# Kernel tuning notes

Hardware: AMD Instinct MI355X
Metric: run time of the kernel (lower is better)

## Reference

```python
import jax, jax.numpy as jnp
import numpy as np

DIM_H = 128
N_EXPERTS = 4
N_GRAPHS = 256
EPS = 1e-5


def setup_inputs() -> dict:
    key = jax.random.key(0)
    ks = jax.random.split(key, 16)
    N, E, D = 100000, 1600000, DIM_H
    x = jax.random.normal(ks[0], (N, D), dtype=jnp.float32)
    edge_index = jax.random.randint(ks[1], (2, E), 0, N, dtype=jnp.int64)
    batch = jnp.sort(jax.random.randint(ks[2], (N,), 0, N_GRAPHS, dtype=jnp.int64))
    s = 0.05
    gin = 2 * D + 4  # router input: mean | max | 4 graph stats
    params = dict(
        temperature=jnp.ones((1,), jnp.float32) * 2.0,
        rw1=jax.random.normal(ks[3], (gin, D), jnp.float32) * s,
        rb1=jnp.zeros((D,), jnp.float32),
        rw2=jax.random.normal(ks[4], (D, D // 2), jnp.float32) * s,
        rb2=jnp.zeros((D // 2,), jnp.float32),
        rw3=jax.random.normal(ks[5], (D // 2, N_EXPERTS), jnp.float32) * s,
        rb3=jnp.zeros((N_EXPERTS,), jnp.float32),
        expert_w=jax.random.normal(ks[6], (N_EXPERTS, D, D), jnp.float32) * s,
        expert_b=jnp.zeros((N_EXPERTS, D), jnp.float32),
        bn1_g=jnp.ones((D,), jnp.float32),
        bn1_b=jnp.zeros((D,), jnp.float32),
        ff_w1=jax.random.normal(ks[7], (D, 2 * D), jnp.float32) * s,
        ff_b1=jnp.zeros((2 * D,), jnp.float32),
        ff_w2=jax.random.normal(ks[8], (2 * D, D), jnp.float32) * s,
        ff_b2=jnp.zeros((D,), jnp.float32),
        bn2_g=jnp.ones((D,), jnp.float32),
        bn2_b=jnp.zeros((D,), jnp.float32),
    )
    return dict(x=x, edge_index=edge_index, batch=batch, **params)


def _gcn_agg(x, src, dst, n):
    deg = jnp.zeros((n,), x.dtype).at[dst].add(1.0) + 1.0
    dinv = jax.lax.rsqrt(deg)
    coef = dinv[src] * dinv[dst]                        # [E]
    agg = jax.ops.segment_sum(x[src] * coef[:, None], dst, num_segments=n)
    return agg + x * (1.0 / deg)[:, None]               # self-loop term (coef = 1/deg)


def _batchnorm(h, g, b):
    mu = jnp.mean(h, axis=0)
    var = jnp.var(h, axis=0)
    return (h - mu) * jax.lax.rsqrt(var + EPS) * g + b


def reference(x, edge_index, batch, temperature, rw1, rb1, rw2, rb2, rw3, rb3,
              expert_w, expert_b, bn1_g, bn1_b, ff_w1, ff_b1, ff_w2, ff_b2,
              bn2_g, bn2_b):
    n = x.shape[0]
    src, dst = edge_index[0], edge_index[1]
    B = N_GRAPHS

    # ---- graph embeddings: [mean_pool | max_pool | 4 stats] -> [B, 2D+4] ----
    cnt = jnp.maximum(jax.ops.segment_sum(jnp.ones((n,), x.dtype), batch, num_segments=B), 1.0)
    gmean = jax.ops.segment_sum(x, batch, num_segments=B) / cnt[:, None]
    gmax = jax.ops.segment_max(x, batch, num_segments=B)
    node_deg = jnp.zeros((n,), x.dtype).at[dst].add(1.0)
    mean_deg = jax.ops.segment_sum(node_deg, batch, num_segments=B) / cnt
    max_deg = jax.ops.segment_max(node_deg, batch, num_segments=B)
    stats = jnp.stack([cnt, mean_deg, max_deg, jnp.log(cnt)], axis=-1)  # [B,4]
    ge = jnp.concatenate([gmean, gmax, stats], axis=-1)

    # ---- router: MLP + temperature softmax -> [B, E] ----
    h = jax.nn.relu(ge @ rw1 + rb1)
    h = jax.nn.relu(h @ rw2 + rb2)
    scores = h @ rw3 + rb3
    gates = jax.nn.softmax(scores / temperature, axis=-1)   # [B, n_experts]

    # ---- experts: GCNConv_i(x). Aggregation is linear so do it once. ----
    agg = _gcn_agg(x, src, dst, n)                          # [N, D]
    expert_out = jnp.einsum('nd,edo->neo', agg, expert_w) + expert_b[None]  # [N,E,D]

    # ---- softmax-gated combine with per-graph gates ----
    kv = jnp.einsum('neo,ne->no', expert_out, gates[batch])  # [N, D]

    # ---- residual + batchnorm + FFN block ----
    kv = _batchnorm(x + kv, bn1_g, bn1_b)
    ff = jax.nn.relu(kv @ ff_w1 + ff_b1) @ ff_w2 + ff_b2
    out = _batchnorm(kv + ff, bn2_g, bn2_b)
    return out
```

## Files before the change

kernel.cpp:

```cpp
#include <hip/hip_runtime.h>
#include <math.h>

#define D 128
#define B 256
#define EPSV 1e-5f
#define NREP 64

typedef __attribute__((ext_vector_type(8))) short short8;
typedef __attribute__((ext_vector_type(4))) float f32x4;

static __device__ __forceinline__ ushort f2bf(float f) {
  union { float f; unsigned u; } v; v.f = f;
  unsigned r = (v.u + 0x7fffu + ((v.u >> 16) & 1u)) >> 16;
  return (ushort)r;
}
static __device__ __forceinline__ float bf2f(ushort u) {
  union { unsigned u; float f; } v; v.u = ((unsigned)u) << 16; return v.f;
}
static __device__ __forceinline__ float uaf(unsigned u) {
  union { unsigned u; float f; } v; v.u = u; return v.f;
}
static __device__ __forceinline__ unsigned encf(float f) {
  union { float f; unsigned u; } v; v.f = f;
  return (v.u & 0x80000000u) ? ~v.u : (v.u | 0x80000000u);
}
static __device__ __forceinline__ float decf(unsigned e) {
  union { unsigned u; float f; } v;
  v.u = (e & 0x80000000u) ? (e & 0x7FFFFFFFu) : ~e;
  return v.f;
}
#define ENC_NEGINF 0x007FFFFFu

static __global__ void __launch_bounds__(256) setup_kernel(
    int* bcnt, float* bn1s, float* bn1s2, float* bn2s, float* bn2s2,
    float* gsum, unsigned* gmaxE, float* gcnt, float* gdsum, unsigned* gdmaxE,
    const float* __restrict__ w1, const float* __restrict__ w2,
    ushort* __restrict__ w1t, ushort* __restrict__ w2t,
    int N, int nbInit) {
  int b = blockIdx.x, t = threadIdx.x;
  if (b < nbInit) {
    int i = b * 256 + t;
    if (i < 256) bcnt[i] = 0;
    if (i < NREP * D) { bn1s[i] = 0.f; bn1s2[i] = 0.f; bn2s[i] = 0.f; bn2s2[i] = 0.f; }
    if (i < B * D) { gsum[i] = 0.f; gmaxE[i] = ENC_NEGINF; }
    if (i < B) { gcnt[i] = 0.f; gdsum[i] = 0.f; gdmaxE[i] = ENC_NEGINF; }
  } else {
    int i = (b - nbInit) * 256 + t;
    { int j = i >> 7, d = i & 127; w1t[i] = f2bf(w1[(size_t)d * 256 + j]); }
    { int o = i >> 8, j = i & 255; w2t[i] = f2bf(w2[(size_t)j * 128 + o]); }
  }
}

static __global__ void __launch_bounds__(256) bhist_kernel(
    const int* __restrict__ dst, int* bcnt, int E) {
  __shared__ int histS[256];
  int t = threadIdx.x;
  int base = blockIdx.x * 4096;
  histS[t] = 0;
  __syncthreads();
#pragma unroll
  for (int k = 0; k < 16; k++) {
    int e = base + k * 256 + t;
    if (e < E) atomicAdd(&histS[dst[e] >> 9], 1);
  }
  __syncthreads();
  int hv = histS[t];
  if (hv > 0) atomicAdd(&bcnt[t], hv);
}

static __global__ void bscan_kernel(const int* __restrict__ bcnt, int* bbase, int* bcur) {
  __shared__ int sS[256];
  int t = threadIdx.x;
  int v = bcnt[t];
  sS[t] = v; __syncthreads();
  for (int off = 1; off < 256; off <<= 1) {
    int add = (t >= off) ? sS[t - off] : 0;
    __syncthreads();
    sS[t] += add;
    __syncthreads();
  }
  int incl = sS[t];
  bbase[t + 1] = incl;
  bcur[t] = incl - v;
  if (t == 0) bbase[0] = 0;
}

static __global__ void statspart_kernel(const float* __restrict__ x, const int* __restrict__ batch,
                                        const float* __restrict__ dinv,
                                        float* gsum, unsigned* gmaxE,
                                        ushort* __restrict__ x_bf, int N) {
  __shared__ float dS[32];
  __shared__ int bSg[32];
  int t = threadIdx.x;
  int n0 = blockIdx.x * 32;
  int nend = min(n0 + 32, N);
  int nn = nend - n0;
  if (t < 32) {
    int n = min(n0 + t, N - 1);
    dS[t] = dinv[n];
    bSg[t] = batch[n];
  }
  __syncthreads();
  float v[32];
#pragma unroll
  for (int k = 0; k < 32; k++)
    v[k] = (k < nn) ? x[(size_t)(n0 + k) * D + t] : 0.f;
#pragma unroll
  for (int k = 0; k < 32; k++)
    if (k < nn) x_bf[(size_t)(n0 + k) * D + t] = f2bf(v[k] * dS[k]);
  int curg = bSg[0];
  float s = 0.f, mx = -INFINITY;
#pragma unroll
  for (int k = 0; k < 32; k++) {
    if (k < nn) {
      int g = bSg[k];
      if (g != curg) {
        atomicAdd(&gsum[curg * D + t], s);
        atomicMax(&gmaxE[curg * D + t], encf(mx));
        s = 0.f; mx = -INFINITY; curg = g;
      }
      s += v[k]; mx = fmaxf(mx, v[k]);
    }
  }
  atomicAdd(&gsum[curg * D + t], s);
  atomicMax(&gmaxE[curg * D + t], encf(mx));
}

static __global__ void router_kernel(
    const float* __restrict__ gsum, const unsigned* __restrict__ gmaxE,
    const float* __restrict__ gcnt, const float* __restrict__ gdsum,
    const unsigned* __restrict__ gdmaxE,
    const float* __restrict__ rw1, const float* __restrict__ rb1,
    const float* __restrict__ rw2, const float* __restrict__ rb2,
    const float* __restrict__ rw3, const float* __restrict__ rb3,
    const float* __restrict__ temp, float* __restrict__ gates) {
  int g = blockIdx.x, t = threadIdx.x;
  __shared__ float geS[260], h1S[D], h2S[64], scS[4];
  float cntf = fmaxf(gcnt[g], 1.f);
  geS[t] = gsum[g * D + t] / cntf;
  geS[D + t] = decf(gmaxE[g * D + t]);
  if (t == 0) {
    geS[256] = cntf;
    geS[257] = gdsum[g] / cntf;
    geS[258] = decf(gdmaxE[g]);
    geS[259] = logf(cntf);
  }
  __syncthreads();
  float a = rb1[t];
  for (int k = 0; k < 260; k++) a += geS[k] * rw1[k * D + t];
  h1S[t] = fmaxf(a, 0.f);
  __syncthreads();
  if (t < 64) { float b = rb2[t]; for (int k = 0; k < D; k++) b += h1S[k] * rw2[k * 64 + t]; h2S[t] = fmaxf(b, 0.f); }
  __syncthreads();
  if (t < 4) { float c = rb3[t]; for (int k = 0; k < 64; k++) c += h2S[k] * rw3[k * 4 + t]; scS[t] = c; }
  __syncthreads();
  if (t == 0) {
    float T = temp[0];
    float q0 = scS[0] / T, q1 = scS[1] / T, q2 = scS[2] / T, q3 = scS[3] / T;
    float m = fmaxf(fmaxf(q0, q1), fmaxf(q2, q3));
    float e0 = expf(q0 - m), e1 = expf(q1 - m), e2 = expf(q2 - m), e3 = expf(q3 - m);
    float inv = 1.f / (e0 + e1 + e2 + e3);
    gates[g * 4 + 0] = e0 * inv; gates[g * 4 + 1] = e1 * inv;
    gates[g * 4 + 2] = e2 * inv; gates[g * 4 + 3] = e3 * inv;
  }
}

static __global__ void __launch_bounds__(256) wcomb_kernel(
    const float* __restrict__ gates, const float* __restrict__ ew,
    const float* __restrict__ eb, ushort* __restrict__ W_combT,
    float* __restrict__ b_comb) {
  __shared__ ushort wS[128 * 130];
  int g = blockIdx.x, t = threadIdx.x;
  float g0 = gates[g * 4], g1 = gates[g * 4 + 1], g2 = gates[g * 4 + 2], g3 = gates[g * 4 + 3];
  for (int k = t; k < D * D; k += 256) {
    int d = k >> 7, o = k & 127;
    float v = g0 * ew[k] + g1 * ew[16384 + k] + g2 * ew[32768 + k] + g3 * ew[49152 + k];
    wS[o * 130 + d] = f2bf(v);
  }
  __syncthreads();
  for (int k = t; k < D * D; k += 256) {
    int o = k >> 7, d = k & 127;
    W_combT[(size_t)g * 16384 + k] = wS[o * 130 + d];
  }
  if (t < D)
    b_comb[g * D + t] = g0 * eb[t] + g1 * eb[D + t] + g2 * eb[2 * D + t] + g3 * eb[3 * D + t];
}

static __global__ void __launch_bounds__(256) fillA_kernel(
    const int* __restrict__ src, const int* __restrict__ dst,
    int* bcur, int* __restrict__ esort, int E) {
  __shared__ int histS[256], startS[256], cursorS[256], gbaseS[256];
  __shared__ int eS[4096];
  __shared__ unsigned char bS[4096];
  int t = threadIdx.x;
  int base = blockIdx.x * 4096;
  int cnt = min(4096, E - base);
  int srcR[16], dstR[16];
  histS[t] = 0;
  __syncthreads();
#pragma unroll
  for (int k = 0; k < 16; k++) {
    int e = base + k * 256 + t;
    if (e < E) { srcR[k] = src[e]; dstR[k] = dst[e]; }
    else dstR[k] = -1;
  }
#pragma unroll
  for (int k = 0; k < 16; k++)
    if (dstR[k] >= 0) atomicAdd(&histS[dstR[k] >> 9], 1);
  __syncthreads();
  int hv = histS[t];
  startS[t] = hv;
  __syncthreads();
  for (int off = 1; off < 256; off <<= 1) {
    int add = (t >= off) ? startS[t - off] : 0;
    __syncthreads();
    startS[t] += add;
    __syncthreads();
  }
  int excl = startS[t] - hv;
  __syncthreads();
  startS[t] = excl;
  cursorS[t] = excl;
  gbaseS[t] = (hv > 0) ? atomicAdd(&bcur[t], hv) : 0;
  __syncthreads();
#pragma unroll
  for (int k = 0; k < 16; k++)
    if (dstR[k] >= 0) {
      int b = dstR[k] >> 9;
      int p = atomicAdd(&cursorS[b], 1);
      eS[p] = (srcR[k] << 9) | (dstR[k] & 511);
      bS[p] = (unsigned char)b;
    }
  __syncthreads();
  for (int k = t; k < cnt; k += 256) {
    int b = bS[k];
    esort[gbaseS[b] + (k - startS[b])] = eS[k];
  }
}

static __global__ void __launch_bounds__(256) fillB_kernel(
    const int* __restrict__ esort, const int* __restrict__ bbase,
    int* __restrict__ rowoff, int* __restrict__ node_deg, float* __restrict__ dinv,
    int* __restrict__ csr_src, int N) {
  __shared__ int degS[512];
  __shared__ int pS[256];
  __shared__ int curS[512];
  int b = blockIdx.x, t = threadIdx.x;
  int n0 = b << 9, n1 = min(n0 + 512, N);
  int nn = n1 - n0;
  int r0 = bbase[b], r1 = bbase[b + 1];
  degS[t] = 0; degS[t + 256] = 0;
  __syncthreads();
  for (int e = r0 + t; e < r1; e += 256) atomicAdd(&degS[esort[e] & 511], 1);
  __syncthreads();
  int d0 = degS[2 * t], d1 = degS[2 * t + 1];
  int ps = d0 + d1;
  pS[t] = ps;
  __syncthreads();
  for (int off = 1; off < 256; off <<= 1) {
    int add = (t >= off) ? pS[t - off] : 0;
    __syncthreads();
    pS[t] += add;
    __syncthreads();
  }
  int pexcl = pS[t] - ps;
  int e0 = pexcl, e1 = pexcl + d0;
  curS[2 * t] = r0 + e0;
  curS[2 * t + 1] = r0 + e1;
  int i0 = 2 * t, i1 = 2 * t + 1;
  if (i0 < nn) {
    rowoff[n0 + i0 + 1] = r0 + e0 + d0;
    node_deg[n0 + i0] = d0;
    dinv[n0 + i0] = rsqrtf((float)d0 + 1.f);
  }
  if (i1 < nn) {
    rowoff[n0 + i1 + 1] = r0 + e1 + d1;
    node_deg[n0 + i1] = d1;
    dinv[n0 + i1] = rsqrtf((float)d1 + 1.f);
  }
  if (b == 0 && t == 0) rowoff[0] = 0;
  __syncthreads();
  for (int e = r0 + t; e < r1; e += 256) {
    int v = esort[e];
    int p = atomicAdd(&curS[v & 511], 1);
    csr_src[p] = v >> 9;
  }
}

static __global__ void nodestats_kernel(const int* __restrict__ node_deg,
                                        const int* __restrict__ batch,
                                        float* gcnt, float* gdsum, unsigned* gdmaxE, int N) {
  int i = blockIdx.x * 256 + threadIdx.x;
  int nd = (i < N) ? node_deg[i] : 0;
  int g = batch[min(i, N - 1)];
  float dv = (float)nd;
  int g0w = __shfl(g, 0);
  int waveLast = blockIdx.x * 256 + ((threadIdx.x >> 6) << 6) + 63;
  bool uni = (waveLast < N) && __all(g == g0w);
  if (uni) {
    float s = dv, mx = dv;
    for (int off = 32; off > 0; off >>= 1) { s += __shfl_down(s, off); mx = fmaxf(mx, __shfl_down(mx, off)); }
    if ((threadIdx.x & 63) == 0) {
      atomicAdd(&gcnt[g0w], 64.f);
      atomicAdd(&gdsum[g0w], s);
      atomicMax(&gdmaxE[g0w], encf(mx));
    }
  } else if (i < N) {
    atomicAdd(&gcnt[g], 1.f);
    atomicAdd(&gdsum[g], dv);
    atomicMax(&gdmaxE[g], encf(dv));
  }
}

static __global__ void __launch_bounds__(256) gather_kernel(
    const ushort* __restrict__ xb, const int* __restrict__ rowoff,
    const int* __restrict__ csr_src, const float* __restrict__ dinv,
    ushort* __restrict__ aggB, int N) {
  __shared__ int eS[4][64];
  int t = threadIdx.x, w = t >> 6, l = t & 63;
  int n = blockIdx.x * 4 + w;
  if (n >= N) return;
  int h = l >> 4;
  int c16 = l & 15;
  int r0 = rowoff[n], r1 = rowoff[n + 1];
  float dn = dinv[n];
  const uint4* xb4 = (const uint4*)xb;
  uint4 xo = xb4[(size_t)n * 16 + c16];
  float acc[8];
#pragma unroll
  for (int i = 0; i < 8; i++) acc[i] = 0.f;
  int pads = 0;
#define ACC8(v) { \
    unsigned u0 = (v).x, u1 = (v).y, u2 = (v).z, u3 = (v).w; \
    acc[0] += uaf(u0 << 16); acc[1] += uaf(u0 & 0xFFFF0000u); \
    acc[2] += uaf(u1 << 16); acc[3] += uaf(u1 & 0xFFFF0000u); \
    acc[4] += uaf(u2 << 16); acc[5] += uaf(u2 & 0xFFFF0000u); \
    acc[6] += uaf(u3 << 16); acc[7] += uaf(u3 & 0xFFFF0000u); }
  for (int j0 = r0; j0 < r1; j0 += 64) {
    int cnt = min(64, r1 - j0);
    int cnt4 = (cnt + 3) & ~3;
    pads += cnt4 - cnt;
    eS[w][l] = (j0 + l < r1) ? csr_src[j0 + l] : n;
    int k = 0;
    for (; k + 16 <= cnt4; k += 16) {
      int s0 = eS[w][k + h];
      int s1 = eS[w][k + 4 + h];
      int s2 = eS[w][k + 8 + h];
      int s3 = eS[w][k + 12 + h];
      uint4 v0 = xb4[(size_t)s0 * 16 + c16];
      uint4 v1 = xb4[(size_t)s1 * 16 + c16];
      uint4 v2 = xb4[(size_t)s2 * 16 + c16];
      uint4 v3 = xb4[(size_t)s3 * 16 + c16];
      ACC8(v0); ACC8(v1); ACC8(v2); ACC8(v3);
    }
    if (k + 8 <= cnt4) {
      int s0 = eS[w][k + h];
      int s1 = eS[w][k + 4 + h];
      uint4 v0 = xb4[(size_t)s0 * 16 + c16];
      uint4 v1 = xb4[(size_t)s1 * 16 + c16];
      ACC8(v0); ACC8(v1);
      k += 8;
    }
    if (k < cnt4) {
      int s0 = eS[w][k + h];
      uint4 v0 = xb4[(size_t)s0 * 16 + c16];
      ACC8(v0);
    }
  }
#undef ACC8
#pragma unroll
  for (int i = 0; i < 8; i++) {
    acc[i] += __shfl_down(acc[i], 32);
    acc[i] += __shfl_down(acc[i], 16);
  }
  if (l < 16) {
    float wn = 1.f - (float)pads;
    float xf[8];
    xf[0] = uaf(xo.x << 16); xf[1] = uaf(xo.x & 0xFFFF0000u);
    xf[2] = uaf(xo.y << 16); xf[3] = uaf(xo.y & 0xFFFF0000u);
    xf[4] = uaf(xo.z << 16); xf[5] = uaf(xo.z & 0xFFFF0000u);
    xf[6] = uaf(xo.w << 16); xf[7] = uaf(xo.w & 0xFFFF0000u);
    unsigned o[4];
#pragma unroll
    for (int i = 0; i < 4; i++) {
      unsigned lo = f2bf(dn * (acc[2 * i] + wn * xf[2 * i]));
      unsigned hi = f2bf(dn * (acc[2 * i + 1] + wn * xf[2 * i + 1]));
      o[i] = lo | (hi << 16);
    }
    uint4 ov; ov.x = o[0]; ov.y = o[1]; ov.z = o[2]; ov.w = o[3];
    ((uint4*)aggB)[(size_t)n * 16 + c16] = ov;
  }
}

static __global__ void __launch_bounds__(256) expert_kernel(
    const ushort* __restrict__ aggB, const float* __restrict__ x, const int* __restrict__ batch,
    const ushort* __restrict__ W_combT, const float* __restrict__ b_comb,
    ushort* __restrict__ hB, float* bn1s, float* bn1s2, int N) {
  __shared__ __align__(16) ushort aggS[64 * 136];
  __shared__ __align__(16) ushort wS[128 * 136];
  __shared__ int bS[64];
  int t = threadIdx.x;
  int nwg = gridDim.x;
  int q = nwg >> 3, r = nwg & 7;
  int xcd = blockIdx.x & 7, ix = blockIdx.x >> 3;
  int tilei = (xcd < r) ? (xcd * (q + 1) + ix) : (r * (q + 1) + (xcd - r) * q + ix);
  int n0 = tilei * 64;
  int tile = min(64, N - n0);
  for (int k = t; k < 64 * 16; k += 256) {
    int i = k >> 4, c = (k & 15) * 8;
    short8 v = (short8){0, 0, 0, 0, 0, 0, 0, 0};
    if (i < tile) v = *(const short8*)&aggB[(size_t)(n0 + i) * D + c];
    *(short8*)&aggS[i * 136 + c] = v;
  }
  if (t < 64) bS[t] = batch[min(n0 + t, N - 1)];
  __syncthreads();
  int w = t >> 6, ln = t & 15, quad = (t & 63) >> 4, l64 = t & 63;
  int myg = bS[l64];
  int gnext = __shfl_down(myg, 1);
  unsigned long long bmask = __ballot(l64 == 63 || myg != gnext);
  float s[2] = {0.f, 0.f}, s2[2] = {0.f, 0.f};
  int mstart = 0;
  while (mstart < tile) {
    int g = __shfl(myg, mstart);
    int mend = mstart + __ffsll((unsigned long long)(bmask >> mstart));
    if (mend > tile) mend = tile;
    __syncthreads();
    const ushort* Wg = W_combT + (size_t)g * 16384;
    for (int k = t; k < 128 * 16; k += 256) {
      int o = k >> 4, c = (k & 15) * 8;
      *(short8*)&wS[o * 136 + c] = *(const short8*)&Wg[(size_t)o * 128 + c];
    }
    __syncthreads();
    f32x4 acc[4][2];
#pragma unroll
    for (int mi = 0; mi < 4; mi++)
#pragma unroll
      for (int ni = 0; ni < 2; ni++) acc[mi][ni] = (f32x4){0.f, 0.f, 0.f, 0.f};
#pragma unroll
    for (int ks = 0; ks < 4; ks++) {
      int kk = ks * 32 + quad * 8;
      short8 a[4], b[2];
#pragma unroll
      for (int mi = 0; mi < 4; mi++) a[mi] = *(const short8*)&aggS[(mi * 16 + ln) * 136 + kk];
#pragma unroll
      for (int ni = 0; ni < 2; ni++) b[ni] = *(const short8*)&wS[(w * 32 + ni * 16 + ln) * 136 + kk];
#pragma unroll
      for (int mi = 0; mi < 4; mi++)
#pragma unroll
        for (int ni = 0; ni < 2; ni++)
          acc[mi][ni] = __builtin_amdgcn_mfma_f32_16x16x32_bf16(a[mi], b[ni], acc[mi][ni], 0, 0, 0);
    }
    float bias[2];
#pragma unroll
    for (int ni = 0; ni < 2; ni++) bias[ni] = b_comb[g * D + w * 32 + ni * 16 + ln];
#pragma unroll
    for (int mi = 0; mi < 4; mi++)
#pragma unroll
      for (int r2_ = 0; r2_ < 4; r2_++) {
        int m = mi * 16 + quad * 4 + r2_;
        if (m >= mstart && m < mend) {
          size_t rowoff_ = (size_t)(n0 + m) * D;
#pragma unroll
          for (int ni = 0; ni < 2; ni++) {
            int o = w * 32 + ni * 16 + ln;
            float hv = x[rowoff_ + o] + acc[mi][ni][r2_] + bias[ni];
            hB[rowoff_ + o] = f2bf(hv);
            s[ni] += hv; s2[ni] += hv * hv;
          }
        }
      }
    mstart = mend;
  }
#pragma unroll
  for (int ni = 0; ni < 2; ni++) {
    s[ni] += __shfl_down(s[ni], 32);  s[ni] += __shfl_down(s[ni], 16);
    s2[ni] += __shfl_down(s2[ni], 32); s2[ni] += __shfl_down(s2[ni], 16);
  }
  if (quad == 0) {
    int slot = (tilei & (NREP - 1)) * D;
#pragma unroll
    for (int ni = 0; ni < 2; ni++) {
      int o = w * 32 + ni * 16 + ln;
      atomicAdd(&bn1s[slot + o], s[ni]);
      atomicAdd(&bn1s2[slot + o], s2[ni]);
    }
  }
}

static __global__ void bnfin_kernel(const float* s, const float* s2,
                                    const float* __restrict__ g, const float* __restrict__ b,
                                    float* sc, float* sh, float invN) {
  int t = threadIdx.x;
  if (t < D) {
    float st = 0.f, s2t = 0.f;
    for (int k = 0; k < NREP; k++) { st += s[k * D + t]; s2t += s2[k * D + t]; }
    float m = st * invN;
    float var = s2t * invN - m * m;
    float rstd = rsqrtf(var + EPSV);
    float scv = rstd * g[t];
    sc[t] = scv;
    sh[t] = b[t] - m * scv;
  }
}

static __global__ void __launch_bounds__(512, 4) ffn_kernel(
    ushort* __restrict__ hB, const float* __restrict__ sc1, const float* __restrict__ sh1,
    const ushort* __restrict__ w1t, const float* __restrict__ fb1,
    const ushort* __restrict__ w2t, const float* __restrict__ fb2,
    float* bn2s, float* bn2s2, int N) {
  __shared__ __align__(16) ushort kvnS[64 * 136];
  __shared__ __align__(16) ushort hidS[64 * 264];
  int t = threadIdx.x, n0 = blockIdx.x * 64;
  int tile = min(64, N - n0);
  for (int k = t; k < 64 * 16; k += 512) {
    int i = k >> 4, c = (k & 15) * 8;
    ushort o[8];
    if (i < tile) {
      uint4 hv = *(const uint4*)&hB[(size_t)(n0 + i) * D + c];
      unsigned uu[4] = {hv.x, hv.y, hv.z, hv.w};
#pragma unroll
      for (int j = 0; j < 4; j++) {
        float lo = uaf(uu[j] << 16) * sc1[c + 2 * j] + sh1[c + 2 * j];
        float hi = uaf(uu[j] & 0xFFFF0000u) * sc1[c + 2 * j + 1] + sh1[c + 2 * j + 1];
        o[2 * j] = f2bf(lo); o[2 * j + 1] = f2bf(hi);
      }
    } else {
#pragma unroll
      for (int j = 0; j < 8; j++) o[j] = 0;
    }
    *(short8*)&kvnS[i * 136 + c] = *(short8*)o;
  }
  __syncthreads();
  int w = t >> 6, ln = t & 15, quad = (t & 63) >> 4;
  f32x4 acc1[4][2];
#pragma unroll
  for (int mi = 0; mi < 4; mi++)
#pragma unroll
    for (int ni = 0; ni < 2; ni++) acc1[mi][ni] = (f32x4){0.f, 0.f, 0.f, 0.f};
#pragma unroll
  for (int ks = 0; ks < 4; ks++) {
    int kk = ks * 32 + quad * 8;
    short8 a[4], b[2];
#pragma unroll
    for (int mi = 0; mi < 4; mi++) a[mi] = *(const short8*)&kvnS[(mi * 16 + ln) * 136 + kk];
#pragma unroll
    for (int ni = 0; ni < 2; ni++) b[ni] = *(const short8*)&w1t[(size_t)(w * 32 + ni * 16 + ln) * 128 + kk];
#pragma unroll
    for (int mi = 0; mi < 4; mi++)
#pragma unroll
      for (int ni = 0; ni < 2; ni++)
        acc1[mi][ni] = __builtin_amdgcn_mfma_f32_16x16x32_bf16(a[mi], b[ni], acc1[mi][ni], 0, 0, 0);
  }
  float bias1[2];
#pragma unroll
  for (int ni = 0; ni < 2; ni++) bias1[ni] = fb1[w * 32 + ni * 16 + ln];
#pragma unroll
  for (int mi = 0; mi < 4; mi++)
#pragma unroll
    for (int ni = 0; ni < 2; ni++)
#pragma unroll
      for (int r = 0; r < 4; r++) {
        int mrow = mi * 16 + quad * 4 + r;
        int j = w * 32 + ni * 16 + ln;
        hidS[mrow * 264 + j] = f2bf(fmaxf(acc1[mi][ni][r] + bias1[ni], 0.f));
      }
  __syncthreads();
  int o = w * 16 + ln;
  f32x4 acc2[4];
#pragma unroll
  for (int mi = 0; mi < 4; mi++) acc2[mi] = (f32x4){0.f, 0.f, 0.f, 0.f};
#pragma unroll
  for (int ks = 0; ks < 8; ks++) {
    int kk = ks * 32 + quad * 8;
    short8 a[4], b;
#pragma unroll
    for (int mi = 0; mi < 4; mi++) a[mi] = *(const short8*)&hidS[(mi * 16 + ln) * 264 + kk];
    b = *(const short8*)&w2t[(size_t)o * 256 + kk];
#pragma unroll
    for (int mi = 0; mi < 4; mi++)
      acc2[mi] = __builtin_amdgcn_mfma_f32_16x16x32_bf16(a[mi], b, acc2[mi], 0, 0, 0);
  }
  float bias2 = fb2[o];
  float s = 0.f, s2 = 0.f;
#pragma unroll
  for (int mi = 0; mi < 4; mi++)
#pragma unroll
    for (int r = 0; r < 4; r++) {
      int mrow = mi * 16 + quad * 4 + r;
      if (mrow < tile) {
        size_t ro = (size_t)(n0 + mrow) * D;
        float v = bf2f(kvnS[mrow * 136 + o]) + acc2[mi][r] + bias2;
        hB[ro + o] = f2bf(v);
        s += v; s2 += v * v;
      }
    }
  s += __shfl_down(s, 32);  s += __shfl_down(s, 16);
  s2 += __shfl_down(s2, 32); s2 += __shfl_down(s2, 16);
  if (quad == 0) {
    int slot = (blockIdx.x & (NREP - 1)) * D;
    atomicAdd(&bn2s[slot + o], s);
    atomicAdd(&bn2s2[slot + o], s2);
  }
}

static __global__ void bnapply_kernel(const ushort* __restrict__ hB, float* __restrict__ out,
                                      const float* __restrict__ sc, const float* __restrict__ sh,
                                      int total8) {
  int i = blockIdx.x * 256 + threadIdx.x;
  if (i < total8) {
    int c = (i * 8) & 127;
    uint4 hv = ((const uint4*)hB)[i];
    unsigned uu[4] = {hv.x, hv.y, hv.z, hv.w};
    float4 o0, o1;
    o0.x = uaf(uu[0] << 16) * sc[c] + sh[c];
    o0.y = uaf(uu[0] & 0xFFFF0000u) * sc[c + 1] + sh[c + 1];
    o0.z = uaf(uu[1] << 16) * sc[c + 2] + sh[c + 2];
    o0.w = uaf(uu[1] & 0xFFFF0000u) * sc[c + 3] + sh[c + 3];
    o1.x = uaf(uu[2] << 16) * sc[c + 4] + sh[c + 4];
    o1.y = uaf(uu[2] & 0xFFFF0000u) * sc[c + 5] + sh[c + 5];
    o1.z = uaf(uu[3] << 16) * sc[c + 6] + sh[c + 6];
    o1.w = uaf(uu[3] & 0xFFFF0000u) * sc[c + 7] + sh[c + 7];
    ((float4*)out)[i * 2] = o0;
    ((float4*)out)[i * 2 + 1] = o1;
  }
}

extern "C" void kernel_launch(void* const* d_in, const int* in_sizes, int n_in,
                              void* d_out, int out_size, void* d_ws, size_t ws_size,
                              hipStream_t stream) {
  (void)n_in; (void)out_size; (void)ws_size;
  const float* x    = (const float*)d_in[0];
  const int*   ei   = (const int*)d_in[1];
  const int*   batch= (const int*)d_in[2];
  const float* temp = (const float*)d_in[3];
  const float* rw1  = (const float*)d_in[4];
  const float* rb1  = (const float*)d_in[5];
  const float* rw2  = (const float*)d_in[6];
  const float* rb2  = (const float*)d_in[7];
  const float* rw3  = (const float*)d_in[8];
  const float* rb3  = (const float*)d_in[9];
  const float* ew   = (const float*)d_in[10];
  const float* eb   = (const float*)d_in[11];
  const float* bn1g = (const float*)d_in[12];
  const float* bn1b = (const float*)d_in[13];
  const float* fw1  = (const float*)d_in[14];
  const float* fb1  = (const float*)d_in[15];
  const float* fw2  = (const float*)d_in[16];
  const float* fb2  = (const float*)d_in[17];
  const float* bn2g = (const float*)d_in[18];
  const float* bn2b = (const float*)d_in[19];

  int N = in_sizes[0] / D;
  int E = in_sizes[1] / 2;
  const int* src = ei;
  const int* dst = ei + E;

  ushort* x_bf = (ushort*)d_out;
  ushort* aggB = (ushort*)((char*)d_out + (size_t)N * D * 2);

  char* p = (char*)d_ws;
  auto alloc = [&](size_t bytes) -> void* {
    void* r = (void*)p;
    p += (bytes + 255) & ~(size_t)255;
    return r;
  };
  int NB = (N + 511) >> 9;
  int*   node_deg = (int*)alloc((size_t)N * 4);
  int*   rowoff   = (int*)alloc(((size_t)N + 1) * 4);
  int*   csr_src  = (int*)alloc((size_t)E * 4);
  int*   esort    = (int*)alloc((size_t)E * 4);
  int*   bcnt     = (int*)alloc(256 * 4);
  int*   bbase    = (int*)alloc(257 * 4);
  int*   bcur     = (int*)alloc(256 * 4);
  float* dinv     = (float*)alloc((size_t)N * 4);
  ushort* hB      = (ushort*)alloc((size_t)N * D * 2);
  float* gsum     = (float*)alloc((size_t)B * D * 4);
  unsigned* gmaxE = (unsigned*)alloc((size_t)B * D * 4);
  float* gcnt     = (float*)alloc((size_t)B * 4);
  float* gdsum    = (float*)alloc((size_t)B * 4);
  unsigned* gdmaxE= (unsigned*)alloc((size_t)B * 4);
  float* gates    = (float*)alloc((size_t)B * 4 * 4);
  float* b_comb   = (float*)alloc((size_t)B * D * 4);
  float* bn1s     = (float*)alloc((size_t)NREP * D * 4);
  float* bn1s2    = (float*)alloc((size_t)NREP * D * 4);
  float* sc1      = (float*)alloc(D * 4);
  float* sh1      = (float*)alloc(D * 4);
  float* bn2s     = (float*)alloc((size_t)NREP * D * 4);
  float* bn2s2    = (float*)alloc((size_t)NREP * D * 4);
  float* sc2      = (float*)alloc(D * 4);
  float* sh2      = (float*)alloc(D * 4);
  ushort* W_combT = (ushort*)alloc((size_t)B * D * D * 2);
  ushort* w1t     = (ushort*)alloc((size_t)D * 256 * 2);
  ushort* w2t     = (ushort*)alloc((size_t)D * 256 * 2);

  int nbInit = (N + 255) / 256;
  setup_kernel<<<nbInit + 128, 256, 0, stream>>>(
      bcnt, bn1s, bn1s2, bn2s, bn2s2, gsum, gmaxE, gcnt, gdsum, gdmaxE,
      fw1, fw2, w1t, w2t, N, nbInit);
  bhist_kernel<<<(E + 4095) / 4096, 256, 0, stream>>>(dst, bcnt, E);
  bscan_kernel<<<1, 256, 0, stream>>>(bcnt, bbase, bcur);
  fillA_kernel<<<(E + 4095) / 4096, 256, 0, stream>>>(src, dst, bcur, esort, E);
  fillB_kernel<<<NB, 256, 0, stream>>>(esort, bbase, rowoff, node_deg, dinv, csr_src, N);
  nodestats_kernel<<<(N + 255) / 256, 256, 0, stream>>>(node_deg, batch, gcnt, gdsum, gdmaxE, N);
  statspart_kernel<<<(N + 31) / 32, 128, 0, stream>>>(x, batch, dinv, gsum, gmaxE, x_bf, N);
  router_kernel<<<B, 128, 0, stream>>>(gsum, gmaxE, gcnt, gdsum, gdmaxE,
                                       rw1, rb1, rw2, rb2, rw3, rb3, temp, gates);
  wcomb_kernel<<<B, 256, 0, stream>>>(gates, ew, eb, W_combT, b_comb);
  gather_kernel<<<(N + 3) / 4, 256, 0, stream>>>(x_bf, rowoff, csr_src, dinv, aggB, N);
  int nb64 = (N + 63) / 64;
  expert_kernel<<<nb64, 256, 0, stream>>>(aggB, x, batch, W_combT, b_comb, hB, bn1s, bn1s2, N);
  bnfin_kernel<<<1, 128, 0, stream>>>(bn1s, bn1s2, bn1g, bn1b, sc1, sh1, 1.0f / (float)N);
  ffn_kernel<<<nb64, 512, 0, stream>>>(hB, sc1, sh1, w1t, fb1, w2t, fb2, bn2s, bn2s2, N);
  bnfin_kernel<<<1, 128, 0, stream>>>(bn2s, bn2s2, bn2g, bn2b, sc2, sh2, 1.0f / (float)N);
  int total8 = N * D / 8;
  bnapply_kernel<<<(total8 + 255) / 256, 256, 0, stream>>>(hB, (float*)d_out, sc2, sh2, total8);
}
```

Measured before the change: 416.7 us.

## Fuse per-graph degree stats into fillB and split FFN hidden into halves

Removes the separate nodestats kernel by computing per-graph count, degree sum and max degree inside fillB, which already holds each node's degree, using wave-level reductions when a wave maps to a single graph. The FFN kernel now processes the 256-wide hidden layer in two 128-column halves, accumulating the second GEMM across halves. This halves the hidden LDS buffer and raises the launch-bounds occupancy target from 4 to 8 blocks, at the cost of an extra barrier per half and possible register pressure.

```diff
diff --git a/kernel.cpp b/kernel.cpp
--- a/kernel.cpp
+++ b/kernel.cpp
@@ -241,7 +241,8 @@
 static __global__ void __launch_bounds__(256) fillB_kernel(
     const int* __restrict__ esort, const int* __restrict__ bbase,
     int* __restrict__ rowoff, int* __restrict__ node_deg, float* __restrict__ dinv,
-    int* __restrict__ csr_src, int N) {
+    int* __restrict__ csr_src, const int* __restrict__ batch,
+    float* gcnt, float* gdsum, unsigned* gdmaxE, int N) {
   __shared__ int degS[512];
   __shared__ int pS[256];
   __shared__ int curS[512];
@@ -279,36 +280,36 @@
     dinv[n0 + i1] = rsqrtf((float)d1 + 1.f);
   }
   if (b == 0 && t == 0) rowoff[0] = 0;
+  {
+    bool v0 = i0 < nn, v1 = i1 < nn;
+    int gn0 = batch[min(n0 + i0, N - 1)];
+    int gn1 = batch[min(n0 + i1, N - 1)];
+    int gfirst = __shfl(gn0, 0);
+    bool uni = __all(gn0 == gfirst) && __all(gn1 == gfirst);
+    if (uni) {
+      float cnt = (v0 ? 1.f : 0.f) + (v1 ? 1.f : 0.f);
+      float sum = (v0 ? (float)d0 : 0.f) + (v1 ? (float)d1 : 0.f);
+      float mx = fmaxf(v0 ? (float)d0 : -INFINITY, v1 ? (float)d1 : -INFINITY);
+      for (int off = 32; off > 0; off >>= 1) {
+        cnt += __shfl_down(cnt, off);
+        sum += __shfl_down(sum, off);
+        mx = fmaxf(mx, __shfl_down(mx, off));
+      }
+      if ((t & 63) == 0 && cnt > 0.f) {
+        atomicAdd(&gcnt[gfirst], cnt);
+        atomicAdd(&gdsum[gfirst], sum);
+        atomicMax(&gdmaxE[gfirst], encf(mx));
+      }
+    } else {
+      if (v0) { atomicAdd(&gcnt[gn0], 1.f); atomicAdd(&gdsum[gn0], (float)d0); atomicMax(&gdmaxE[gn0], encf((float)d0)); }
+      if (v1) { atomicAdd(&gcnt[gn1], 1.f); atomicAdd(&gdsum[gn1], (float)d1); atomicMax(&gdmaxE[gn1], encf((float)d1)); }
+    }
+  }
   __syncthreads();
   for (int e = r0 + t; e < r1; e += 256) {
     int v = esort[e];
     int p = atomicAdd(&curS[v & 511], 1);
     csr_src[p] = v >> 9;
-  }
-}
-
-static __global__ void nodestats_kernel(const int* __restrict__ node_deg,
-                                        const int* __restrict__ batch,
-                                        float* gcnt, float* gdsum, unsigned* gdmaxE, int N) {
-  int i = blockIdx.x * 256 + threadIdx.x;
-  int nd = (i < N) ? node_deg[i] : 0;
-  int g = batch[min(i, N - 1)];
-  float dv = (float)nd;
-  int g0w = __shfl(g, 0);
-  int waveLast = blockIdx.x * 256 + ((threadIdx.x >> 6) << 6) + 63;
-  bool uni = (waveLast < N) && __all(g == g0w);
-  if (uni) {
-    float s = dv, mx = dv;
-    for (int off = 32; off > 0; off >>= 1) { s += __shfl_down(s, off); mx = fmaxf(mx, __shfl_down(mx, off)); }
-    if ((threadIdx.x & 63) == 0) {
-      atomicAdd(&gcnt[g0w], 64.f);
-      atomicAdd(&gdsum[g0w], s);
-      atomicMax(&gdmaxE[g0w], encf(mx));
-    }
-  } else if (i < N) {
-    atomicAdd(&gcnt[g], 1.f);
-    atomicAdd(&gdsum[g], dv);
-    atomicMax(&gdmaxE[g], encf(dv));
   }
 }
 
@@ -503,13 +504,13 @@
   }
 }
 
-static __global__ void __launch_bounds__(512, 4) ffn_kernel(
+static __global__ void __launch_bounds__(512, 8) ffn_kernel(
     ushort* __restrict__ hB, const float* __restrict__ sc1, const float* __restrict__ sh1,
     const ushort* __restrict__ w1t, const float* __restrict__ fb1,
     const ushort* __restrict__ w2t, const float* __restrict__ fb2,
     float* bn2s, float* bn2s2, int N) {
   __shared__ __align__(16) ushort kvnS[64 * 136];
-  __shared__ __align__(16) ushort hidS[64 * 264];
+  __shared__ __align__(16) ushort hidS[64 * 136];
   int t = threadIdx.x, n0 = blockIdx.x * 64;
   int tile = min(64, N - n0);
   for (int k = t; k < 64 * 16; k += 512) {
@@ -532,53 +533,47 @@
   }
   __syncthreads();
   int w = t >> 6, ln = t & 15, quad = (t & 63) >> 4;
-  f32x4 acc1[4][2];
-#pragma unroll
-  for (int mi = 0; mi < 4; mi++)
-#pragma unroll
-    for (int ni = 0; ni < 2; ni++) acc1[mi][ni] = (f32x4){0.f, 0.f, 0.f, 0.f};
-#pragma unroll
-  for (int ks = 0; ks < 4; ks++) {
-    int kk = ks * 32 + quad * 8;
-    short8 a[4], b[2];
-#pragma unroll
-    for (int mi = 0; mi < 4; mi++) a[mi] = *(const short8*)&kvnS[(mi * 16 + ln) * 136 + kk];
-#pragma unroll
-    for (int ni = 0; ni < 2; ni++) b[ni] = *(const short8*)&w1t[(size_t)(w * 32 + ni * 16 + ln) * 128 + kk];
+  int o = w * 16 + ln;
+  f32x4 acc2[4];
+#pragma unroll
+  for (int mi = 0; mi < 4; mi++) acc2[mi] = (f32x4){0.f, 0.f, 0.f, 0.f};
+#pragma unroll
+  for (int half = 0; half < 2; half++) {
+    f32x4 acc1[4];
+#pragma unroll
+    for (int mi = 0; mi < 4; mi++) acc1[mi] = (f32x4){0.f, 0.f, 0.f, 0.f};
+#pragma unroll
+    for (int ks = 0; ks < 4; ks++) {
+      int kk = ks * 32 + quad * 8;
+      short8 a[4], b;
+#pragma unroll
+      for (int mi = 0; mi < 4; mi++) a[mi] = *(const short8*)&kvnS[(mi * 16 + ln) * 136 + kk];
+      b = *(const short8*)&w1t[(size_t)(half * 128 + o) * 128 + kk];
+#pragma unroll
+      for (int mi = 0; mi < 4; mi++)
+        acc1[mi] = __builtin_amdgcn_mfma_f32_16x16x32_bf16(a[mi], b, acc1[mi], 0, 0, 0);
+    }
+    float bias1 = fb1[half * 128 + o];
+    if (half == 1) __syncthreads();
 #pragma unroll
     for (int mi = 0; mi < 4; mi++)
-#pragma unroll
-      for (int ni = 0; ni < 2; ni++)
-        acc1[mi][ni] = __builtin_amdgcn_mfma_f32_16x16x32_bf16(a[mi], b[ni], acc1[mi][ni], 0, 0, 0);
-  }
-  float bias1[2];
-#pragma unroll
-  for (int ni = 0; ni < 2; ni++) bias1[ni] = fb1[w * 32 + ni * 16 + ln];
-#pragma unroll
-  for (int mi = 0; mi < 4; mi++)
-#pragma unroll
-    for (int ni = 0; ni < 2; ni++)
 #pragma unroll
       for (int r = 0; r < 4; r++) {
         int mrow = mi * 16 + quad * 4 + r;
-        int j = w * 32 + ni * 16 + ln;
-        hidS[mrow * 264 + j] = f2bf(fmaxf(acc1[mi][ni][r] + bias1[ni], 0.f));
+        hidS[mrow * 136 + o] = f2bf(fmaxf(acc1[mi][r] + bias1, 0.f));
       }
-  __syncthreads();
-  int o = w * 16 + ln;
-  f32x4 acc2[4];
-#pragma unroll
-  for (int mi = 0; mi < 4; mi++) acc2[mi] = (f32x4){0.f, 0.f, 0.f, 0.f};
-#pragma unroll
-  for (int ks = 0; ks < 8; ks++) {
-    int kk = ks * 32 + quad * 8;
-    short8 a[4], b;
-#pragma unroll
-    for (int mi = 0; mi < 4; mi++) a[mi] = *(const short8*)&hidS[(mi * 16 + ln) * 264 + kk];
-    b = *(const short8*)&w2t[(size_t)o * 256 + kk];
-#pragma unroll
-    for (int mi = 0; mi < 4; mi++)
-      acc2[mi] = __builtin_amdgcn_mfma_f32_16x16x32_bf16(a[mi], b, acc2[mi], 0, 0, 0);
+    __syncthreads();
+#pragma unroll
+    for (int ks = 0; ks < 4; ks++) {
+      int kk = ks * 32 + quad * 8;
+      short8 a[4], b;
+#pragma unroll
+      for (int mi = 0; mi < 4; mi++) a[mi] = *(const short8*)&hidS[(mi * 16 + ln) * 136 + kk];
+      b = *(const short8*)&w2t[(size_t)o * 256 + half * 128 + kk];
+#pragma unroll
+      for (int mi = 0; mi < 4; mi++)
+        acc2[mi] = __builtin_amdgcn_mfma_f32_16x16x32_bf16(a[mi], b, acc2[mi], 0, 0, 0);
+    }
   }
   float bias2 = fb2[o];
   float s = 0.f, s2 = 0.f;
@@ -700,8 +695,8 @@
   bhist_kernel<<<(E + 4095) / 4096, 256, 0, stream>>>(dst, bcnt, E);
   bscan_kernel<<<1, 256, 0, stream>>>(bcnt, bbase, bcur);
   fillA_kernel<<<(E + 4095) / 4096, 256, 0, stream>>>(src, dst, bcur, esort, E);
-  fillB_kernel<<<NB, 256, 0, stream>>>(esort, bbase, rowoff, node_deg, dinv, csr_src, N);
-  nodestats_kernel<<<(N + 255) / 256, 256, 0, stream>>>(node_deg, batch, gcnt, gdsum, gdmaxE, N);
+  fillB_kernel<<<NB, 256, 0, stream>>>(esort, bbase, rowoff, node_deg, dinv, csr_src,
+                                       batch, gcnt, gdsum, gdmaxE, N);
   statspart_kernel<<<(N + 31) / 32, 128, 0, stream>>>(x, batch, dinv, gsum, gmaxE, x_bf, N);
   router_kernel<<<B, 128, 0, stream>>>(gsum, gmaxE, gcnt, gdsum, gdmaxE,
                                        rw1, rb1, rw2, rb2, rw3, rb3, temp, gates);
```

Result: slower. 437.1 us (+4.9%).
